# Kernel optimization log

Measured on AMD Instinct MI355X. Metric: run time of the kernel, lower is better.

## Reference

```python
import jax, jax.numpy as jnp
import numpy as np

CTX = 2048
D_IN = 2048
D_OUT = 2048
N_HEADS = 16
HEAD_DIM = D_OUT // N_HEADS
ROPE_BASE = 10000.0


def rope_tables(head_dim, ctx):
    inv_freq = 1.0 / (ROPE_BASE ** (jnp.arange(0, head_dim, 2, dtype=jnp.float32) / head_dim))
    angles = jnp.arange(ctx, dtype=jnp.float32)[:, None] * inv_freq[None, :]  # [ctx, hd/2]
    angles = jnp.concatenate([angles, angles], axis=1)  # [ctx, hd]
    return jnp.sin(angles), jnp.cos(angles)


def apply_rope(x, sin, cos):
    # x: [b, h, s, d]; rotate-by-half (Raschka / Llama style)
    s = x.shape[2]
    d = x.shape[3]
    x1, x2 = x[..., : d // 2], x[..., d // 2 :]
    rotated = jnp.concatenate([-x2, x1], axis=-1)
    return x * cos[:s][None, None] + rotated * sin[:s][None, None]


def setup_inputs() -> dict:
    key = jax.random.key(0)
    kx, kq, kk, kv, ko = jax.random.split(key, 5)
    scale = 0.02
    return {
        "x": jax.random.normal(kx, (2, CTX, D_IN), dtype=jnp.float32),
        "W_query": jax.random.normal(kq, (D_IN, D_OUT), dtype=jnp.float32) * scale,
        "W_key": jax.random.normal(kk, (D_IN, D_OUT), dtype=jnp.float32) * scale,
        "W_value": jax.random.normal(kv, (D_IN, D_OUT), dtype=jnp.float32) * scale,
        "W_out": jax.random.normal(ko, (D_OUT, D_OUT), dtype=jnp.float32) * scale,
    }


def reference(x, W_query, W_key, W_value, W_out):
    bs, cl, _ = x.shape
    sin, cos = rope_tables(HEAD_DIM, CTX)

    def split_heads(t):  # [b, s, d_out] -> [b, h, s, hd]
        return t.reshape(bs, cl, N_HEADS, HEAD_DIM).transpose(0, 2, 1, 3)

    q = split_heads(x @ W_query)
    k = split_heads(x @ W_key)
    v = split_heads(x @ W_value)

    q = apply_rope(q, sin, cos)
    k = apply_rope(k, sin, cos)

    # NOTE: original module does NOT scale by 1/sqrt(head_dim)
    scores = jnp.einsum("bhqd,bhkd->bhqk", q, k)
    causal = jnp.triu(jnp.ones((cl, cl), dtype=bool), k=1)
    scores = jnp.where(causal[None, None], -jnp.inf, scores)
    weights = jax.nn.softmax(scores, axis=-1)
    ctx = jnp.einsum("bhqk,bhkd->bhqd", weights, v)
    ctx = ctx.transpose(0, 2, 1, 3).reshape(bs, cl, N_HEADS * HEAD_DIM)
    return ctx @ W_out
```

## Files before the change

### kernel.cpp

```cpp
#include <hip/hip_runtime.h>
#include <cstdint>
#include <cstddef>

typedef _Float16 f16;
typedef _Float16 f16x8 __attribute__((ext_vector_type(8)));
typedef _Float16 f16x4 __attribute__((ext_vector_type(4)));
typedef float    f32x4 __attribute__((ext_vector_type(4)));
typedef float    f32x16 __attribute__((ext_vector_type(16)));
typedef int      i32x4 __attribute__((ext_vector_type(4)));

#define S_CTX 2048
#define NH 16
#define DH 128

#define BAR() asm volatile("s_barrier" ::: "memory")
#define VMW(n) asm volatile("s_waitcnt vmcnt(" #n ")" ::: "memory")
#define MF(a, b, c) __builtin_amdgcn_mfma_f32_16x16x32_f16((a), (b), (c), 0, 0, 0)
#define MF32(a, b, c) __builtin_amdgcn_mfma_f32_32x32x16_f16((a), (b), (c), 0, 0, 0)

__device__ __forceinline__ void gload16(const void* g, void* l) {
  __builtin_amdgcn_global_load_lds(
      (const __attribute__((address_space(1))) void*)g,
      (__attribute__((address_space(3))) void*)l, 16, 0, 0);
}

__device__ __forceinline__ int pk2(float a, float b) {
  auto hv = __builtin_amdgcn_cvt_pkrtz(a, b);
  return __builtin_bit_cast(int, hv);
}
__device__ __forceinline__ void pl_swap(int& a, int& b) {
  asm volatile("v_permlane32_swap_b32 %0, %1" : "+v"(a), "+v"(b));
}

__global__ void prep(const float* __restrict__ x,
                     const float* __restrict__ w0, const float* __restrict__ w1,
                     const float* __restrict__ w2, const float* __restrict__ w3,
                     f16* __restrict__ xb,
                     f16* __restrict__ o0, f16* __restrict__ o1,
                     f16* __restrict__ o2, f16* __restrict__ o3,
                     float* __restrict__ sint, float* __restrict__ cost) {
  const int bid = blockIdx.x, tid = threadIdx.x;
  if (bid < 512) {
    int idx = bid * 256 + tid;
    int j = idx & 63, s = idx >> 6;
    float invf = __expf(-(float)(2 * j) * (1.0f / 128.0f) * 9.210340371976184f);
    float a = (float)s * invf;
    sint[idx] = sinf(a);
    cost[idx] = cosf(a);
  } else if (bid < 8704) {
    int i = ((bid - 512) * 256 + tid) * 4;
    float4 v = *(const float4*)(x + i);
    f16x4 o; o[0] = (f16)v.x; o[1] = (f16)v.y; o[2] = (f16)v.z; o[3] = (f16)v.w;
    *(f16x4*)(xb + i) = o;
  } else {
    int b2 = bid - 8704;
    int z = b2 >> 12, rem = b2 & 4095;
    int by = rem >> 6, bx = rem & 63;
    int tx = tid & 31, ty = tid >> 5;
    const float* in; f16* out;
    switch (z) {
      case 0: in = w0; out = o0; break;
      case 1: in = w1; out = o1; break;
      case 2: in = w2; out = o2; break;
      default: in = w3; out = o3; break;
    }
    __shared__ float tl[32][33];
    int xc = bx * 32 + tx, yc = by * 32 + ty;
#pragma unroll
    for (int r = 0; r < 32; r += 8)
      tl[ty + r][tx] = in[(size_t)(yc + r) * 2048 + xc];
    __syncthreads();
    int xo = by * 32 + tx, yo = bx * 32 + ty;
#pragma unroll
    for (int r = 0; r < 32; r += 8)
      out[(size_t)(yo + r) * 2048 + xo] = (f16)tl[tx][ty + r];
  }
}

__global__ __launch_bounds__(512, 1)
void gemm_qk(const f16* __restrict__ A, const f16* __restrict__ wqT,
             const f16* __restrict__ wkT,
             f16* __restrict__ qb, f16* __restrict__ kb,
             const float* __restrict__ sint, const float* __restrict__ cost) {
  extern __shared__ __align__(16) char lds[];
  const int tid = threadIdx.x, lane = tid & 63;
  const int wvi = tid >> 6, wm = wvi >> 2, wn = wvi & 3;
  const int gcol = blockIdx.x * 256;
  const int proj = gcol >> 11;
  const int col0 = gcol & 2047;
  const int row0 = blockIdx.y * 256;
  const f16* Bt = proj ? wkT : wqT;

  const int ca0 = tid, ca1 = tid + 512;
  const int ra0 = ca0 >> 2, ra1 = ca1 >> 2;
  const int sa0 = (ca0 & 3) ^ ((ra0 >> 1) & 3);
  const int sa1 = (ca1 & 3) ^ ((ra1 >> 1) & 3);
  const f16* gA0 = A + (size_t)(row0 + ra0) * 2048 + sa0 * 8;
  const f16* gA1 = A + (size_t)(row0 + ra1) * 2048 + sa1 * 8;
  const f16* gB0 = Bt + (size_t)(col0 + ra0) * 2048 + sa0 * 8;
  const f16* gB1 = Bt + (size_t)(col0 + ra1) * 2048 + sa1 * 8;

  const int kslot = lane >> 4;
  int aoff[8], boff[4];
#pragma unroll
  for (int i = 0; i < 8; i++) {
    int row = wm * 128 + i * 16 + (lane & 15);
    aoff[i] = row * 64 + ((kslot ^ ((row >> 1) & 3)) << 4);
  }
#pragma unroll
  for (int j = 0; j < 4; j++) {
    int rb = (wn >> 1) * 128 + (wn & 1) * 32 + (j & 1) * 16 + (j >> 1) * 64 + (lane & 15);
    boff[j] = rb * 64 + ((kslot ^ ((rb >> 1) & 3)) << 4);
  }

  f32x4 acc[8][4] = {};

#define QKPH(SLOT, HS, SSLOT, DOSTAGE, WN) do {                                \
    const char* As_ = lds + (SLOT) * 32768;                                    \
    const char* Bs_ = As_ + 16384;                                             \
    f16x8 af[8], bf[4];                                                        \
    _Pragma("unroll") for (int i_ = 0; i_ < 8; i_++)                           \
      af[i_] = *(const f16x8*)(As_ + aoff[i_]);                                \
    _Pragma("unroll") for (int j_ = 0; j_ < 4; j_++)                           \
      bf[j_] = *(const f16x8*)(Bs_ + boff[j_]);                                \
    if (DOSTAGE) {                                                             \
      char* dA = lds + (SSLOT) * 32768;                                        \
      gload16(gA0 + (HS) * 32, dA + ca0 * 16);                                 \
      gload16(gA1 + (HS) * 32, dA + ca1 * 16);                                 \
      gload16(gB0 + (HS) * 32, dA + 16384 + ca0 * 16);                         \
      gload16(gB1 + (HS) * 32, dA + 16384 + ca1 * 16);                         \
    }                                                                          \
    asm volatile("s_waitcnt vmcnt(" #WN ")" ::: "memory");                     \
    BAR();                                                                     \
    __builtin_amdgcn_s_setprio(1);                                             \
    _Pragma("unroll") for (int i_ = 0; i_ < 8; i_++)                           \
      _Pragma("unroll") for (int j_ = 0; j_ < 4; j_++)                         \
        acc[i_][j_] = MF(af[i_], bf[j_], acc[i_][j_]);                         \
    __builtin_amdgcn_s_setprio(0);                                             \
    BAR();                                                                     \
  } while (0)

#pragma unroll
  for (int h = 0; h < 3; h++) {
    char* dA = lds + h * 32768;
    gload16(gA0 + h * 32, dA + ca0 * 16);
    gload16(gA1 + h * 32, dA + ca1 * 16);
    gload16(gB0 + h * 32, dA + 16384 + ca0 * 16);
    gload16(gB1 + h * 32, dA + 16384 + ca1 * 16);
  }
  VMW(8); BAR();

  for (int t = 0; t < 15; ++t) {
    const int p = 4 * t;
    QKPH(0, p + 3, 3, 1, 8);
    QKPH(1, p + 4, 0, 1, 8);
    QKPH(2, p + 5, 1, 1, 8);
    QKPH(3, p + 6, 2, 1, 8);
  }
  QKPH(0, 63, 3, 1, 8);
  QKPH(1, 0, 0, 0, 4);
  QKPH(2, 0, 0, 0, 0);
  QKPH(3, 0, 0, 0, 63);
#undef QKPH

  const int b = row0 >> 11, sb = row0 & 2047;
  f16* dst = proj ? kb : qb;
  const int h = (col0 >> 7) + (wn >> 1);
#pragma unroll
  for (int i = 0; i < 8; i++)
#pragma unroll
    for (int jj = 0; jj < 2; jj++)
#pragma unroll
      for (int r = 0; r < 4; r++) {
        int s = sb + wm * 128 + i * 16 + (lane >> 4) * 4 + r;
        int d = (wn & 1) * 32 + jj * 16 + (lane & 15);
        float cv = cost[s * 64 + d], sv = sint[s * 64 + d];
        float x1 = acc[i][jj][r], x2 = acc[i][jj + 2][r];
        size_t base = ((size_t)(b * NH + h) * S_CTX + s) << 7;
        dst[base + d]      = (f16)(x1 * cv - x2 * sv);
        dst[base + d + 64] = (f16)(x2 * cv + x1 * sv);
      }
}

template<int MODE>
__global__ __launch_bounds__(512, 1)
void gemm8(const f16* __restrict__ A, const f16* __restrict__ Bt,
           f16* __restrict__ vtb, float* __restrict__ of) {
  extern __shared__ __align__(16) char lds[];
#define RING_A(e) (lds + (e) * 16384)
#define RING_B(e) (lds + 65536 + (e) * 8192)
  const int tid = threadIdx.x, lane = tid & 63;
  const int wvi = tid >> 6, wm = wvi >> 1, wn = wvi & 1;
  const int col0 = blockIdx.x * 128;
  const int row0 = blockIdx.y * 256;

  const int ca0 = tid, ca1 = tid + 512, cb0 = tid;
  const int rAs0 = ca0 >> 2, rAs1 = ca1 >> 2, rBs0 = cb0 >> 2;
  const int sA0 = (ca0 & 3) ^ ((rAs0 >> 1) & 3);
  const int sA1 = (ca1 & 3) ^ ((rAs1 >> 1) & 3);
  const int sB0 = (cb0 & 3) ^ ((rBs0 >> 1) & 3);
  const f16* gA0 = A + (size_t)(row0 + rAs0) * 2048 + sA0 * 8;
  const f16* gA1 = A + (size_t)(row0 + rAs1) * 2048 + sA1 * 8;
  const f16* gB0 = Bt + (size_t)(col0 + rBs0) * 2048 + sB0 * 8;

  const int kslot = lane >> 4;
  int aoff[4], boff[4];
#pragma unroll
  for (int i = 0; i < 4; i++) {
    int row = wm * 64 + i * 16 + (lane & 15);
    aoff[i] = row * 64 + ((kslot ^ ((row >> 1) & 3)) << 4);
  }
#pragma unroll
  for (int j = 0; j < 4; j++) {
    int rb = wn * 32 + (j & 1) * 16 + (j >> 1) * 64 + (lane & 15);
    boff[j] = rb * 64 + ((kslot ^ ((rb >> 1) & 3)) << 4);
  }

  f32x4 acc[4][4] = {};

#define PH8(SLOT, HS, DOSTAGE, WN) do {                                        \
    const char* As_ = RING_A(SLOT);                                            \
    const char* Bs_ = RING_B(SLOT);                                            \
    f16x8 af[4], bf[4];                                                        \
    _Pragma("unroll") for (int i_ = 0; i_ < 4; i_++)                           \
      af[i_] = *(const f16x8*)(As_ + aoff[i_]);                                \
    _Pragma("unroll") for (int j_ = 0; j_ < 4; j_++)                           \
      bf[j_] = *(const f16x8*)(Bs_ + boff[j_]);                                \
    if (DOSTAGE) {                                                             \
      gload16(gA0 + (HS) * 32, RING_A((HS) & 3) + ca0 * 16);                   \
      gload16(gA1 + (HS) * 32, RING_A((HS) & 3) + ca1 * 16);                   \
      gload16(gB0 + (HS) * 32, RING_B((HS) & 3) + cb0 * 16);                   \
    }                                                                          \
    asm volatile("s_waitcnt vmcnt(" #WN ")" ::: "memory");                     \
    BAR();                                                                     \
    __builtin_amdgcn_s_setprio(1);                                             \
    _Pragma("unroll") for (int i_ = 0; i_ < 4; i_++)                           \
      _Pragma("unroll") for (int j_ = 0; j_ < 4; j_++)                         \
        acc[i_][j_] = MF(af[i_], bf[j_], acc[i_][j_]);                         \
    __builtin_amdgcn_s_setprio(0);                                             \
    BAR();                                                                     \
  } while (0)

#pragma unroll
  for (int h = 0; h < 3; h++) {
    gload16(gA0 + h * 32, RING_A(h) + ca0 * 16);
    gload16(gA1 + h * 32, RING_A(h) + ca1 * 16);
    gload16(gB0 + h * 32, RING_B(h) + cb0 * 16);
  }
  VMW(6); BAR();

  for (int t = 0; t < 15; ++t) {
    const int p = t * 4;
    PH8(0, p + 3, 1, 6);
    PH8(1, p + 4, 1, 6);
    PH8(2, p + 5, 1, 6);
    PH8(3, p + 6, 1, 6);
  }
  PH8(0, 63, 1, 6);
  PH8(1, 0, 0, 3);
  PH8(2, 0, 0, 0);
  PH8(3, 0, 0, 63);
#undef PH8

  const int b = row0 >> 11, sbase = row0 & 2047;

  if (MODE == 2) {
#pragma unroll
    for (int i = 0; i < 4; i++)
#pragma unroll
      for (int j = 0; j < 4; j++)
#pragma unroll
        for (int r = 0; r < 4; r++) {
          int row = row0 + wm * 64 + i * 16 + (lane >> 4) * 4 + r;
          int col = col0 + wn * 32 + (j & 1) * 16 + (j >> 1) * 64 + (lane & 15);
          of[(size_t)row * 2048 + col] = acc[i][j][r];
        }
  } else {
    const int h = col0 >> 7;
    f16x4* ldsv = (f16x4*)lds;
#pragma unroll
    for (int i = 0; i < 4; i++)
#pragma unroll
      for (int j = 0; j < 4; j++) {
        f16x4 v;
#pragma unroll
        for (int r = 0; r < 4; r++) v[r] = (f16)acc[i][j][r];
        int su = wm * 16 + i * 4 + (lane >> 4);
        int d  = wn * 32 + (j & 1) * 16 + (j >> 1) * 64 + (lane & 15);
        ldsv[d * 64 + (su ^ ((d << 1) & 63))] = v;
      }
    __syncthreads();
#pragma unroll
    for (int it = 0; it < 8; ++it) {
      int o = it * 512 + tid;
      int d = o >> 5, c = o & 31;
      int xc = (d << 1) & 63;
      f16x4 lo = ldsv[d * 64 + ((2 * c) ^ xc)];
      f16x4 hi = ldsv[d * 64 + ((2 * c + 1) ^ xc)];
      f16x8 vv;
      vv[0] = lo[0]; vv[1] = lo[1]; vv[2] = lo[2]; vv[3] = lo[3];
      vv[4] = hi[0]; vv[5] = hi[1]; vv[6] = hi[2]; vv[7] = hi[3];
      *(f16x8*)&vtb[((size_t)(b * NH + h) * DH + d) * S_CTX + sbase + c * 8] = vv;
    }
  }
#undef RING_A
#undef RING_B
}

__global__ __launch_bounds__(512, 1)
void attn_k(const f16* __restrict__ q, const f16* __restrict__ kk,
            const f16* __restrict__ vt, f16* __restrict__ ctx) {
  extern __shared__ __align__(16) char alds[];
  const int tid = threadIdx.x, lane = tid & 63;
  const int halfid = tid >> 8;
  const int tid2 = tid & 255;
  const int wv2 = tid2 >> 6;
  const int lh = lane >> 5, q31 = lane & 31;
  const int bid = blockIdx.x;
  const int bh = (bid & 7) + 8 * ((bid >> 3) & 3);
  const int idxQ = bid >> 5;
  const int b = bh >> 4, h = bh & 15;
  const size_t plane = (size_t)bh * (S_CTX * DH);
  const f16* Qp = q + plane;
  const f16* Kp = kk + plane;
  const f16* Vp = vt + plane;
  const float LOG2E = 1.4426950408889634f;

  char* myH = alds + halfid * 65536;
  float* O_lds = (float*)(alds + 65536);
  float* ml_lds = (float*)alds;

#define STAGE(T, BUF) do {                                                      \
    const f16* Kt = Kp + (size_t)(T) * 64 * DH;                                 \
    const f16* Vt = Vp + (size_t)(T) * 64;                                      \
    char* kb_ = myH + (BUF) * 16384;                                            \
    char* vb_ = myH + 32768 + (BUF) * 16384;                                    \
    _Pragma("unroll") for (int j_ = 0; j_ < 4; j_++) {                          \
      int c = tid2 + j_ * 256; int rk = c >> 4;                                 \
      gload16(Kt + (size_t)rk * DH + (((c & 15) ^ (rk & 7)) * 8), kb_ + c * 16); \
    }                                                                           \
    _Pragma("unroll") for (int j_ = 0; j_ < 4; j_++) {                          \
      int c = tid2 + j_ * 256; int rv = c >> 3;                                 \
      gload16(Vt + (size_t)rv * S_CTX + (((c & 7) ^ (rv & 7)) * 8), vb_ + c * 16); \
    }                                                                           \
  } while (0)

  for (int p = 0; p < 2; ++p) {
    const int Qt = p ? (15 - idxQ) : idxQ;
    const int q0 = Qt * 128;
    const int NTh = Qt + 1;

    f16x8 qf[8];
    {
      const f16* qq = Qp + (size_t)(q0 + wv2 * 32 + q31) * DH + lh * 8;
#pragma unroll
      for (int s = 0; s < 8; s++) {
        qf[s] = *(const f16x8*)(qq + s * 16);
#pragma unroll
        for (int e = 0; e < 8; e++) qf[s][e] = (f16)((float)qf[s][e] * LOG2E);
      }
    }
    float m_ = -3e38f, l_ = 0.f;
    f32x16 o[4] = {};

    STAGE(halfid, 0);
    VMW(0); BAR();

    int cur = 0;
    for (int i = 0; i < NTh; i++) {
      const int t = 2 * i + halfid;
      if (i + 1 < NTh) STAGE(2 * (i + 1) + halfid, cur ^ 1);
      const f16* Ksc = (const f16*)(myH + cur * 16384);
      const f16* Vsc = (const f16*)(myH + 32768 + cur * 16384);

      f32x16 st0 = {}, st1 = {};
      __builtin_amdgcn_s_setprio(1);
#pragma unroll
      for (int s = 0; s < 8; s++) {
        const int r0 = q31, r1 = 32 + q31;
        f16x8 kf0 = *(const f16x8*)&Ksc[r0 * 128 + (((2 * s + lh) ^ (r0 & 7)) << 3)];
        f16x8 kf1 = *(const f16x8*)&Ksc[r1 * 128 + (((2 * s + lh) ^ (r1 & 7)) << 3)];
        st0 = MF32(kf0, qf[s], st0);
        st1 = MF32(kf1, qf[s], st1);
      }
      __builtin_amdgcn_s_setprio(0);

      if (t >= 2 * Qt) {
        const int qg = q0 + wv2 * 32 + q31;
#pragma unroll
        for (int r = 0; r < 16; r++) {
          int kvb = t * 64 + (r & 3) + 8 * (r >> 2) + 4 * lh;
          if (kvb > qg) st0[r] = -3e38f;
          if (kvb + 32 > qg) st1[r] = -3e38f;
        }
      }
      float mx = st0[0];
#pragma unroll
      for (int r = 1; r < 16; r++) mx = fmaxf(mx, st0[r]);
#pragma unroll
      for (int r = 0; r < 16; r++) mx = fmaxf(mx, st1[r]);
      mx = fmaxf(mx, __shfl_xor(mx, 32));
      if (__any(mx > m_ + 8.0f)) {
        float nm = fmaxf(m_, mx);
        float al = __builtin_amdgcn_exp2f(m_ - nm);
        m_ = nm; l_ *= al;
#pragma unroll
        for (int r = 0; r < 16; r++) {
          float alr = __shfl(al, (r & 3) + 8 * (r >> 2) + 4 * lh);
#pragma unroll
          for (int j = 0; j < 4; j++) o[j][r] *= alr;
        }
      }
      float s_ = 0.f;
#pragma unroll
      for (int r = 0; r < 16; r++) { st0[r] = __builtin_amdgcn_exp2f(st0[r] - m_); s_ += st0[r]; }
#pragma unroll
      for (int r = 0; r < 16; r++) { st1[r] = __builtin_amdgcn_exp2f(st1[r] - m_); s_ += st1[r]; }
      s_ += __shfl_xor(s_, 32);
      l_ += s_;

      f16x8 pa[4];
      {
        int w0 = pk2(st0[0], st0[1]),   w1 = pk2(st0[2], st0[3]);
        int w2 = pk2(st0[4], st0[5]),   w3 = pk2(st0[6], st0[7]);
        int w4 = pk2(st0[8], st0[9]),   w5 = pk2(st0[10], st0[11]);
        int w6 = pk2(st0[12], st0[13]), w7 = pk2(st0[14], st0[15]);
        pl_swap(w0, w2); pl_swap(w1, w3); pl_swap(w4, w6); pl_swap(w5, w7);
        i32x4 a = {w0, w1, w2, w3}; pa[0] = __builtin_bit_cast(f16x8, a);
        i32x4 bb = {w4, w5, w6, w7}; pa[1] = __builtin_bit_cast(f16x8, bb);
      }
      {
        int w0 = pk2(st1[0], st1[1]),   w1 = pk2(st1[2], st1[3]);
        int w2 = pk2(st1[4], st1[5]),   w3 = pk2(st1[6], st1[7]);
        int w4 = pk2(st1[8], st1[9]),   w5 = pk2(st1[10], st1[11]);
        int w6 = pk2(st1[12], st1[13]), w7 = pk2(st1[14], st1[15]);
        pl_swap(w0, w2); pl_swap(w1, w3); pl_swap(w4, w6); pl_swap(w5, w7);
        i32x4 a = {w0, w1, w2, w3}; pa[2] = __builtin_bit_cast(f16x8, a);
        i32x4 bb = {w4, w5, w6, w7}; pa[3] = __builtin_bit_cast(f16x8, bb);
      }

      __builtin_amdgcn_s_setprio(1);
#pragma unroll
      for (int j = 0; j < 4; j++) {
        const int rv = 32 * j + q31;
#pragma unroll
        for (int s2 = 0; s2 < 4; s2++) {
          f16x8 vf = *(const f16x8*)&Vsc[rv * 64 + (((2 * s2 + lh) ^ (rv & 7)) << 3)];
          o[j] = MF32(pa[s2], vf, o[j]);
        }
      }
      __builtin_amdgcn_s_setprio(0);

      VMW(0); BAR();
      cur ^= 1;
    }

    if (halfid) {
      ml_lds[(wv2 * 32 + q31) * 2]     = m_;
      ml_lds[(wv2 * 32 + q31) * 2 + 1] = l_;
#pragma unroll
      for (int r = 0; r < 16; r++) {
        int crow = (r & 3) + 8 * (r >> 2) + 4 * lh;
#pragma unroll
        for (int j = 0; j < 4; j++)
          O_lds[(wv2 * 32 + crow) * 128 + 32 * j + q31] = o[j][r];
      }
    }
    BAR();
    if (!halfid) {
      float mB = ml_lds[(wv2 * 32 + q31) * 2];
      float lB = ml_lds[(wv2 * 32 + q31) * 2 + 1];
      float m = fmaxf(m_, mB);
      float aA = __builtin_amdgcn_exp2f(m_ - m);
      float aB = __builtin_amdgcn_exp2f(mB - m);
      float lfin = l_ * aA + lB * aB;
      float inv = 1.0f / lfin;
#pragma unroll
      for (int r = 0; r < 16; r++) {
        int crow = (r & 3) + 8 * (r >> 2) + 4 * lh;
        float aAr = __shfl(aA, crow);
        float aBr = __shfl(aB, crow);
        float invr = __shfl(inv, crow);
        int qg = q0 + wv2 * 32 + crow;
#pragma unroll
        for (int j = 0; j < 4; j++) {
          float ov = o[j][r] * aAr + O_lds[(wv2 * 32 + crow) * 128 + 32 * j + q31] * aBr;
          ctx[((size_t)(b * S_CTX + qg) * 2048) + h * 128 + 32 * j + q31] = (f16)(ov * invr);
        }
      }
    }
    BAR();
  }
#undef STAGE
}

extern "C" void kernel_launch(void* const* d_in, const int* in_sizes, int n_in,
                              void* d_out, int out_size, void* d_ws, size_t ws_size,
                              hipStream_t stream) {
  (void)in_sizes; (void)n_in; (void)out_size; (void)ws_size;
  const float* x  = (const float*)d_in[0];
  const float* Wq = (const float*)d_in[1];
  const float* Wk = (const float*)d_in[2];
  const float* Wv = (const float*)d_in[3];
  const float* Wo = (const float*)d_in[4];
  float* out = (float*)d_out;
  char* ws = (char*)d_ws;

  f16*   xb   = (f16*)(ws);
  f16*   ctxb = (f16*)(ws);
  f16*   wqT  = (f16*)(ws + 16777216);
  f16*   wkT  = (f16*)(ws + 25165824);
  f16*   wvT  = (f16*)(ws + 33554432);
  f16*   woT  = (f16*)(ws + 41943040);
  f16*   qb   = (f16*)(ws + 50331648);
  f16*   kb   = (f16*)(ws + 67108864);
  f16*   vtb  = (f16*)(ws + 83886080);
  float* sint = (float*)(ws + 100663296);
  float* cost = (float*)(ws + 101187584);

  prep<<<dim3(25088), dim3(256), 0, stream>>>(x, Wq, Wk, Wv, Wo, xb,
                                              wqT, wkT, wvT, woT, sint, cost);
  gemm_qk<<<dim3(16, 16), dim3(512), 131072, stream>>>(xb, wqT, wkT, qb, kb, sint, cost);
  gemm8<1><<<dim3(16, 16), dim3(512), 98304, stream>>>(xb, wvT, vtb, nullptr);
  attn_k<<<dim3(256), dim3(512), 131072, stream>>>(qb, kb, vtb, ctxb);
  gemm8<2><<<dim3(16, 16), dim3(512), 98304, stream>>>(ctxb, woT, nullptr, out);
}
```

Measured before the change: 241.6 us.

## Split QK GEMM k-steps into half-M phases with separate A/B LDS rings

Restructures the QK projection GEMM main loop so each k-slice is processed in two phases, one per half of the M tile. A and B now live in separate LDS rings, and the A and B global-to-LDS loads are issued in alternate phases. The B fragments are cached in registers across the two phases, and vmcnt waits happen every other phase. The goal is to interleave loads and MFMAs at finer grain and spread out load issue, at the cost of more barriers per k-step.

```diff
diff --git a/kernel.cpp b/kernel.cpp
--- a/kernel.cpp
+++ b/kernel.cpp
@@ -83,6 +83,8 @@
              f16* __restrict__ qb, f16* __restrict__ kb,
              const float* __restrict__ sint, const float* __restrict__ cost) {
   extern __shared__ __align__(16) char lds[];
+#define RING_A(e) (lds + (e) * 16384)
+#define RING_B(e) (lds + 65536 + (e) * 16384)
   const int tid = threadIdx.x, lane = tid & 63;
   const int wvi = tid >> 6, wm = wvi >> 2, wn = wvi & 3;
   const int gcol = blockIdx.x * 256;
@@ -114,54 +116,61 @@
   }
 
   f32x4 acc[8][4] = {};
-
-#define QKPH(SLOT, HS, SSLOT, DOSTAGE, WN) do {                                \
-    const char* As_ = lds + (SLOT) * 32768;                                    \
-    const char* Bs_ = As_ + 16384;                                             \
-    f16x8 af[8], bf[4];                                                        \
-    _Pragma("unroll") for (int i_ = 0; i_ < 8; i_++)                           \
-      af[i_] = *(const f16x8*)(As_ + aoff[i_]);                                \
-    _Pragma("unroll") for (int j_ = 0; j_ < 4; j_++)                           \
-      bf[j_] = *(const f16x8*)(Bs_ + boff[j_]);                                \
-    if (DOSTAGE) {                                                             \
-      char* dA = lds + (SSLOT) * 32768;                                        \
-      gload16(gA0 + (HS) * 32, dA + ca0 * 16);                                 \
-      gload16(gA1 + (HS) * 32, dA + ca1 * 16);                                 \
-      gload16(gB0 + (HS) * 32, dA + 16384 + ca0 * 16);                         \
-      gload16(gB1 + (HS) * 32, dA + 16384 + ca1 * 16);                         \
-    }                                                                          \
-    asm volatile("s_waitcnt vmcnt(" #WN ")" ::: "memory");                     \
-    BAR();                                                                     \
-    __builtin_amdgcn_s_setprio(1);                                             \
-    _Pragma("unroll") for (int i_ = 0; i_ < 8; i_++)                           \
-      _Pragma("unroll") for (int j_ = 0; j_ < 4; j_++)                         \
-        acc[i_][j_] = MF(af[i_], bf[j_], acc[i_][j_]);                         \
-    __builtin_amdgcn_s_setprio(0);                                             \
-    BAR();                                                                     \
-  } while (0)
+  f16x8 bfc[4];
+
+  auto PH = [&](int e, int mh, int stagemat, int h) {
+    const char* As_ = RING_A(e);
+    const char* Bs_ = RING_B(e);
+    f16x8 af[4];
+#pragma unroll
+    for (int ii = 0; ii < 4; ii++)
+      af[ii] = *(const f16x8*)(As_ + aoff[mh * 4 + ii]);
+    if (mh == 0) {
+#pragma unroll
+      for (int j = 0; j < 4; j++)
+        bfc[j] = *(const f16x8*)(Bs_ + boff[j]);
+    }
+    if (stagemat == 0) {
+      gload16(gA0 + h * 32, RING_A(h & 3) + ca0 * 16);
+      gload16(gA1 + h * 32, RING_A(h & 3) + ca1 * 16);
+    } else if (stagemat == 1) {
+      gload16(gB0 + h * 32, RING_B(h & 3) + ca0 * 16);
+      gload16(gB1 + h * 32, RING_B(h & 3) + ca1 * 16);
+    }
+    BAR();
+    __builtin_amdgcn_s_setprio(1);
+#pragma unroll
+    for (int j = 0; j < 4; j++)
+#pragma unroll
+      for (int ii = 0; ii < 4; ii++)
+        acc[mh * 4 + ii][j] = MF(af[ii], bfc[j], acc[mh * 4 + ii][j]);
+    __builtin_amdgcn_s_setprio(0);
+  };
 
 #pragma unroll
   for (int h = 0; h < 3; h++) {
-    char* dA = lds + h * 32768;
-    gload16(gA0 + h * 32, dA + ca0 * 16);
-    gload16(gA1 + h * 32, dA + ca1 * 16);
-    gload16(gB0 + h * 32, dA + 16384 + ca0 * 16);
-    gload16(gB1 + h * 32, dA + 16384 + ca1 * 16);
+    gload16(gA0 + h * 32, RING_A(h) + ca0 * 16);
+    gload16(gA1 + h * 32, RING_A(h) + ca1 * 16);
+    gload16(gB0 + h * 32, RING_B(h) + ca0 * 16);
+    gload16(gB1 + h * 32, RING_B(h) + ca1 * 16);
   }
   VMW(8); BAR();
 
-  for (int t = 0; t < 15; ++t) {
-    const int p = 4 * t;
-    QKPH(0, p + 3, 3, 1, 8);
-    QKPH(1, p + 4, 0, 1, 8);
-    QKPH(2, p + 5, 1, 1, 8);
-    QKPH(3, p + 6, 2, 1, 8);
-  }
-  QKPH(0, 63, 3, 1, 8);
-  QKPH(1, 0, 0, 0, 4);
-  QKPH(2, 0, 0, 0, 0);
-  QKPH(3, 0, 0, 0, 63);
-#undef QKPH
+  for (int t = 0; t < 30; ++t) {
+    int e0 = (2 * t) & 3, e1 = (2 * t + 1) & 3;
+    PH(e0, 0, 0, 2 * t + 3);          BAR();
+    PH(e0, 1, 1, 2 * t + 3); VMW(8);  BAR();
+    PH(e1, 0, 0, 2 * t + 4);          BAR();
+    PH(e1, 1, 1, 2 * t + 4); VMW(8);  BAR();
+  }
+  PH(0, 0, 0, 63);          BAR();
+  PH(0, 1, 1, 63); VMW(8);  BAR();
+  PH(1, 0, 2, 0);           BAR();
+  PH(1, 1, 2, 0);  VMW(4);  BAR();
+  PH(2, 0, 2, 0);           BAR();
+  PH(2, 1, 2, 0);  VMW(0);  BAR();
+  PH(3, 0, 2, 0);           BAR();
+  PH(3, 1, 2, 0);           BAR();
 
   const int b = row0 >> 11, sb = row0 & 2047;
   f16* dst = proj ? kb : qb;
@@ -180,6 +189,8 @@
         dst[base + d]      = (f16)(x1 * cv - x2 * sv);
         dst[base + d + 64] = (f16)(x2 * cv + x1 * sv);
       }
+#undef RING_A
+#undef RING_B
 }
 
 template<int MODE>
```

After: 243.5 us. Within noise of the previous version (+0.8%).
